# Optimization experiments

Measured on AMD Instinct MI355X. Metric: run time of the kernel, lower is better.

Reference implementation:

```python
import jax
import jax.numpy as jnp
import numpy as np

B, IN_DIM, OUT_DIM, N = 64, 1024, 512, 2048
LEAKY_SLOPE = 0.01


def apply_nl(idx, x):
    # NONLINEARITY_MAP: 0 ReLU, 1 Tanh, 2 LeakyReLU, 3 Identity, 4 Sine, 5 Softplus, 6 SoftMinus
    branches = [
        lambda v: jax.nn.relu(v),
        lambda v: jnp.tanh(v),
        lambda v: jnp.where(v >= 0, v, LEAKY_SLOPE * v),
        lambda v: v,
        lambda v: jnp.sin(v),
        lambda v: jax.nn.softplus(v),
        lambda v: -jax.nn.softplus(-v),
    ]
    return jax.lax.switch(idx, branches, x)


def setup_inputs() -> dict:
    key = jax.random.key(0)
    ks = jax.random.split(key, 8)
    X = jax.random.normal(ks[0], (B, IN_DIM), dtype=jnp.float32)
    adj = jax.random.randint(ks[1], (N, N), 0, 2).astype(bool)
    nl_idx = jax.random.randint(ks[2], (N,), 0, 7).astype(jnp.int32)
    # kaiming-normal-ish init (std = sqrt(2/fan_in)), bias std 0.1
    W0 = jax.random.normal(ks[3], (IN_DIM, N), dtype=jnp.float32) * np.sqrt(2.0 / IN_DIM)
    b0 = jax.random.normal(ks[4], (N,), dtype=jnp.float32) * 0.1
    W_mid = jax.random.normal(ks[5], (N, N), dtype=jnp.float32) * np.sqrt(2.0 / N)
    b_mid = jax.random.normal(ks[6], (N,), dtype=jnp.float32) * 0.1
    W_out = jax.random.normal(ks[7], (N, OUT_DIM), dtype=jnp.float32) * np.sqrt(2.0 / N)
    b_out = jax.random.normal(jax.random.fold_in(key, 99), (OUT_DIM,), dtype=jnp.float32) * 0.1
    return {"X": X, "adj": adj, "nl_idx": nl_idx, "W0": W0, "b0": b0,
            "W_mid": W_mid, "b_mid": b_mid, "W_out": W_out, "b_out": b_out}


def reference(X, adj, nl_idx, W0, b0, W_mid, b_mid, W_out, b_out):
    n_nodes = adj.shape[0]
    adjf = adj.astype(X.dtype)
    # node 0: Linear(input_dim, adj[0].sum()) + nonlinearity, scattered into state at adj[0]
    out0 = apply_nl(nl_idx[0], X @ W0 + b0)            # [B, N]
    state = jnp.where(adj[0][None, :], out0, jnp.zeros((), X.dtype))  # [B, N]

    # middle nodes 1..N-2: gather state[:, adj[:,n]] -> Linear(.,1) -> nonlinearity -> state[:,n]
    # gather+Linear == masked dot with full-length weight column
    def step(state, n):
        w = W_mid[:, n] * adjf[:, n]                   # [N]
        val = state @ w + b_mid[n]                     # [B]
        val = apply_nl(nl_idx[n], val)
        state = state.at[:, n].set(val)
        return state, None

    nodes = jnp.arange(1, n_nodes - 1)
    state, _ = jax.lax.scan(step, state, nodes)

    # final node: Linear(inputs.sum(), output_dim) + nonlinearity on state[:, adj[:,-1]]
    Wm = W_out * adjf[:, -1][:, None]                  # [N, OUT_DIM] masked
    out = apply_nl(nl_idx[-1], state @ Wm + b_out)     # [B, OUT_DIM]
    return out, state
```

## Files before the change

### kernel.cpp

```cpp
#include <hip/hip_runtime.h>
#include <math.h>

#define BN 64
#define KIN 1024
#define DOUT 512
#define NN 2048
#define TBLK 128
#define NBLK 16

__device__ __forceinline__ float softplus_f(float x) {
  float e = __expf(-fabsf(x));
  return fmaxf(x, 0.f) + __logf(1.f + e);
}
__device__ __forceinline__ float apply_nl(int id, float v) {
  switch (id) {
    case 0: return fmaxf(v, 0.f);
    case 1: { float e = __expf(2.f * v); return fmaf(-2.f, __builtin_amdgcn_rcpf(e + 1.f), 1.f); }
    case 2: return v >= 0.f ? v : 0.01f * v;
    case 3: return v;
    case 4: return __sinf(v);
    case 5: return softplus_f(v);
    default: return v - softplus_f(v);
  }
}

__device__ __forceinline__ void nl_cand(float v, float& mx, float& th, float& lk,
                                        float& sn, float& sp, float& sm) {
  mx = fmaxf(v, 0.f);
  lk = fmaf(fminf(v, 0.f), 0.01f, mx);
  float e = __expf(-fabsf(v));
  float e2 = e * e;
  float l1 = __logf(1.f + e);
  sp = mx + l1;
  sm = v - sp;
  th = __builtin_copysignf((1.f - e2) * __builtin_amdgcn_rcpf(1.f + e2), v);
  sn = __sinf(v);
}
__device__ __forceinline__ float nl_sel(int id, float v, float mx, float th, float lk,
                                        float sn, float sp, float sm) {
  float r = v;
  r = (id == 0) ? mx : r;
  r = (id == 1) ? th : r;
  r = (id == 2) ? lk : r;
  r = (id == 4) ? sn : r;
  r = (id == 5) ? sp : r;
  r = (id == 6) ? sm : r;
  return r;
}

#define TWEL(tw, m, l) (((l) & 3) == 0 ? tw[(m)*2 + ((l) >> 2)].x : \
                        ((l) & 3) == 1 ? tw[(m)*2 + ((l) >> 2)].y : \
                        ((l) & 3) == 2 ? tw[(m)*2 + ((l) >> 2)].z : tw[(m)*2 + ((l) >> 2)].w)

__global__ void detect_adj(const unsigned int* __restrict__ a, int* __restrict__ flags) {
  int idx = blockIdx.x * 256 + threadIdx.x;
  unsigned int v = a[idx];
  bool bad = ((v & 0xFFu) > 1u) || (((v >> 8) & 0xFFu) > 1u) ||
             (((v >> 16) & 0xFFu) > 1u) || ((v >> 24) > 1u);
  bool off = (v & 0xFFFFFF00u) != 0u;
  if (__any(bad) && (threadIdx.x & 63) == 0) atomicOr(&flags[0], 1);
  if (__any(off) && (threadIdx.x & 63) == 0) atomicOr(&flags[1], 1);
}

__global__ void normalize_adj(const unsigned char* __restrict__ a,
                              const int* __restrict__ flags,
                              unsigned char* __restrict__ out) {
  size_t i = (size_t)blockIdx.x * blockDim.x + threadIdx.x;
  int mode = flags[0] ? 2 : (flags[1] ? 1 : 0);
  unsigned char r;
  if (mode == 1)      r = (a[i] != 0);
  else if (mode == 0) r = (((const int*)a)[i] != 0);
  else                r = (((const float*)a)[i] != 0.f);
  out[i] = r;
}

__global__ void transpose_x(const float* __restrict__ X, float* __restrict__ XT) {
  int g = blockIdx.x * blockDim.x + threadIdx.x;
  int k = g >> 6, b = g & 63;
  XT[g] = X[(size_t)b * KIN + k];
}

__global__ __launch_bounds__(256) void pack_wmid(const float* __restrict__ Wmid,
                                                 const unsigned char* __restrict__ adjN,
                                                 float* __restrict__ wpack) {
  int g = blockIdx.x * 256 + threadIdx.x;
  int i = g >> 12;
  int rem = g & 4095;
  int j = rem >> 5;
  int q4 = (rem & 31) * 4;
  int n0 = 1 + i * TBLK;
  int size = NN - 1 - n0;
  if (size > TBLK) size = TBLK;
  float w[4];
#pragma unroll
  for (int e = 0; e < 4; ++e) {
    int q = q4 + e;
    float v = 0.f;
    if (q > j && j < size && q < size) {
      size_t idx = (size_t)(n0 + j) * NN + (size_t)(n0 + q);
      v = Wmid[idx] * (float)adjN[idx];
    }
    w[e] = v;
  }
  *(float4*)(wpack + (size_t)g * 4) = make_float4(w[0], w[1], w[2], w[3]);
}

template <int MODE>
__global__ __launch_bounds__(256) void gemm_partial(
    const float* __restrict__ AT, const float* __restrict__ W,
    const unsigned char* __restrict__ adj, float* __restrict__ accT,
    int ldw, int col0, int ncols, int kPerChunk, int nColTiles)
{
  const int ct = blockIdx.x % nColTiles;
  const int kc = blockIdx.x / nColTiles;
  const int c0 = ct * 64;
  const int k0 = kc * kPerChunk;
  const int t = threadIdx.x;
  const int tb = t >> 4;
  const int tc = t & 15;

  __shared__ __align__(16) float At[16][64];
  __shared__ __align__(16) float Wt[16][64];

  float acc[4][4] = {};
  const int sk = t >> 4;
  const int sq = t & 15;

  for (int ks = k0; ks < k0 + kPerChunk; ks += 16) {
    const float4 av = *(const float4*)(AT + (size_t)(ks + sk) * 64 + sq * 4);
    *(float4*)(&At[sk][sq * 4]) = av;
    {
      const float* wrow = W + (size_t)(ks + sk) * ldw + col0;
      float w[4];
      float rowmask = 1.f;
      if (MODE == 2) rowmask = (float)adj[(size_t)(ks + sk) * NN + (NN - 1)];
#pragma unroll
      for (int e = 0; e < 4; ++e) {
        int cl = c0 + sq * 4 + e;
        float wv = 0.f;
        if (cl < ncols) {
          wv = wrow[cl];
          if (MODE == 1) wv *= (float)adj[(size_t)(ks + sk) * NN + col0 + cl];
          if (MODE == 2) wv *= rowmask;
        }
        w[e] = wv;
      }
      *(float4*)(&Wt[sk][sq * 4]) = make_float4(w[0], w[1], w[2], w[3]);
    }
    __syncthreads();
#pragma unroll
    for (int kk = 0; kk < 16; ++kk) {
      float a4[4], w4[4];
#pragma unroll
      for (int e = 0; e < 4; ++e) a4[e] = At[kk][tb * 4 + e];
#pragma unroll
      for (int e = 0; e < 4; ++e) w4[e] = Wt[kk][tc * 4 + e];
#pragma unroll
      for (int i = 0; i < 4; ++i)
#pragma unroll
        for (int j = 0; j < 4; ++j) acc[i][j] = fmaf(a4[i], w4[j], acc[i][j]);
    }
    __syncthreads();
  }

#pragma unroll
  for (int j = 0; j < 4; ++j) {
    int cl = c0 + tc * 4 + j;
    if (cl < ncols) {
      float* dst = accT + (size_t)(col0 + cl) * 64 + tb * 4;
#pragma unroll
      for (int i = 0; i < 4; ++i) atomicAdd(dst + i, acc[i][j]);
    }
  }
}

__global__ void init_finish(const float* __restrict__ out0accT, const float* __restrict__ b0,
                            const unsigned char* __restrict__ adjN, const int* __restrict__ nl_idx,
                            float* __restrict__ curT) {
  int g = blockIdx.x * blockDim.x + threadIdx.x;
  int n = g >> 6;
  float v = out0accT[g] + b0[n];
  v = apply_nl(nl_idx[0], v);
  curT[g] = adjN[n] ? v : 0.f;
}

__global__ __launch_bounds__(256, 1) void fused_solve(
    const float* __restrict__ wpack, const float* __restrict__ Wmid,
    const unsigned char* __restrict__ adjN, const int* __restrict__ nlidx,
    const float* __restrict__ bmid, const float* __restrict__ Cbase,
    float* __restrict__ curT, float* __restrict__ deltaG, int* solveDone)
{
  __shared__ __align__(16) unsigned char smem[132096];
  float (*wmS)[TBLK]     = (float(*)[TBLK])(smem);
  float (*wpr)[TBLK]     = (float(*)[TBLK])(smem + 65536);
  float (*deltaFull)[64] = (float(*)[64])(smem + 65536);
  int* idS               = (int*)(smem + 131072);
  int* sfl               = (int*)(smem + 131584);

  const int bi = blockIdx.x;
  const int n0 = 1 + bi * TBLK;
  int size = NN - 1 - n0;
  if (size > TBLK) size = TBLK;
  const int tid = threadIdx.x;
  const int wv = tid >> 6;
  const int b = tid & 63;
  const int qbase = wv * 32;

  {
    const float4* src = (const float4*)(wpack + (size_t)bi * TBLK * TBLK);
    float4 s0[8];
#pragma unroll
    for (int it = 0; it < 8; ++it) s0[it] = src[it * 256 + tid];
#pragma unroll
    for (int it = 0; it < 8; ++it) ((float4*)&wmS[0][0])[it * 256 + tid] = s0[it];
#pragma unroll
    for (int it = 0; it < 8; ++it) s0[it] = src[(8 + it) * 256 + tid];
#pragma unroll
    for (int it = 0; it < 8; ++it) ((float4*)&wmS[0][0])[(8 + it) * 256 + tid] = s0[it];
  }
  if (tid < TBLK) idS[tid] = (tid < size) ? nlidx[n0 + tid] : 3;

  float val[32], iv[32];
#pragma unroll
  for (int l = 0; l < 32; ++l) {
    int q = qbase + l, n = n0 + q;
    bool ok = q < size;
    val[l] = ok ? (Cbase[(size_t)n * 64 + b] + bmid[n]) : 0.f;
    iv[l] = ok ? curT[(size_t)n * 64 + b] : 0.f;
  }
  __syncthreads();

#pragma unroll 1
  for (int p = 0; p < bi; ++p) {
    {
      const size_t rowg0 = (size_t)(1 + p * TBLK);
#pragma unroll 1
      for (int it = 0; it < 16; ++it) {
        int idx = it * 256 + tid;
        int r = idx >> 5, c4 = (idx & 31) * 4;
        const float* wrow = Wmid + (rowg0 + r) * NN + n0;
        const unsigned char* arow = adjN + (rowg0 + r) * NN + n0;
        float w[4];
#pragma unroll
        for (int e = 0; e < 4; ++e) {
          int cl = c4 + e;
          w[e] = (cl < size && arow[cl]) ? wrow[cl] : 0.f;
        }
        *(float4*)(&wpr[r][c4]) = make_float4(w[0], w[1], w[2], w[3]);
      }
    }
    {
      int done = 0, cnt = 0;
      while (!done && cnt < 4000000) {
        if (tid == 0) *sfl = atomicAdd(&solveDone[p], 0);
        __syncthreads();
        done = *sfl;
        __syncthreads();
        ++cnt;
        if (!done) __builtin_amdgcn_s_sleep(2);
      }
    }
    __threadfence();
    const float* dsrc = deltaG + (size_t)p * TBLK * 64 + b;
#pragma unroll 1
    for (int kc = 0; kc < 8; ++kc) {
      float d[16];
#pragma unroll
      for (int k = 0; k < 16; ++k) d[k] = dsrc[(size_t)(kc * 16 + k) * 64];
#pragma unroll
      for (int k = 0; k < 16; ++k) {
        const float4* wr = (const float4*)(&wpr[kc * 16 + k][qbase]);
#pragma unroll
        for (int g2 = 0; g2 < 8; ++g2) {
          float4 w4 = wr[g2];
          val[g2 * 4 + 0] = fmaf(d[k], w4.x, val[g2 * 4 + 0]);
          val[g2 * 4 + 1] = fmaf(d[k], w4.y, val[g2 * 4 + 1]);
          val[g2 * 4 + 2] = fmaf(d[k], w4.z, val[g2 * 4 + 2]);
          val[g2 * 4 + 3] = fmaf(d[k], w4.w, val[g2 * 4 + 3]);
        }
      }
    }
    __syncthreads();
  }

#pragma unroll 1
  for (int c = 0; c < 4; ++c) {
    if (wv == c) {
      const int jbase = c * 32;
      float cmx, cth, clk, csn, csp, csm;
      nl_cand(val[0], cmx, cth, clk, csn, csp, csm);
      int idv = idS[jbase];
#pragma unroll
      for (int s = 0; s < 4; ++s) {
        float4 tw[16];
#pragma unroll
        for (int m = 0; m < 8; ++m) {
          const float4* tr = (const float4*)(&wmS[jbase + s * 8 + m][qbase + s * 8]);
          tw[m * 2] = tr[0];
          tw[m * 2 + 1] = tr[1];
        }
        float ds[8];
#pragma unroll
        for (int m = 0; m < 8; ++m) {
          const int jj = s * 8 + m;
          const int j = jbase + jj;
          float nv = nl_sel(idv, val[jj], cmx, cth, clk, csn, csp, csm);
          float delta = (j < size) ? (nv - iv[jj]) : 0.f;
          ds[m] = delta;
          deltaFull[j][b] = delta;
          if (jj < 31) idv = idS[jbase + jj + 1];
          if (m < 7) {
            val[s * 8 + m + 1] = fmaf(delta, TWEL(tw, m, m + 1), val[s * 8 + m + 1]);
            nl_cand(val[s * 8 + m + 1], cmx, cth, clk, csn, csp, csm);
#pragma unroll
            for (int l = m + 2; l < 8; ++l)
              val[s * 8 + l] = fmaf(delta, TWEL(tw, m, l), val[s * 8 + l]);
          }
        }
        if (s < 3) {
#pragma unroll
          for (int lg = (s + 1) * 2; lg < 8; ++lg) {
#pragma unroll
            for (int m = 0; m < 8; ++m) {
              const float4 w4 = *(const float4*)(&wmS[jbase + s * 8 + m][qbase + lg * 4]);
              val[lg * 4 + 0] = fmaf(ds[m], w4.x, val[lg * 4 + 0]);
              val[lg * 4 + 1] = fmaf(ds[m], w4.y, val[lg * 4 + 1]);
              val[lg * 4 + 2] = fmaf(ds[m], w4.z, val[lg * 4 + 2]);
              val[lg * 4 + 3] = fmaf(ds[m], w4.w, val[lg * 4 + 3]);
            }
            if (lg == (s + 1) * 2)
              nl_cand(val[(s + 1) * 8], cmx, cth, clk, csn, csp, csm);
          }
        }
      }
    }
    __syncthreads();
    if (wv > c) {
#pragma unroll 1
      for (int jj = 0; jj < 32; ++jj) {
        const int j = c * 32 + jj;
        const float delta = deltaFull[j][b];
        const float4* wr = (const float4*)(&wmS[j][qbase]);
        float4 w0 = wr[0], w1 = wr[1], w2 = wr[2], w3 = wr[3];
        float4 w4 = wr[4], w5 = wr[5], w6 = wr[6], w7 = wr[7];
        val[0] = fmaf(delta, w0.x, val[0]);   val[1] = fmaf(delta, w0.y, val[1]);
        val[2] = fmaf(delta, w0.z, val[2]);   val[3] = fmaf(delta, w0.w, val[3]);
        val[4] = fmaf(delta, w1.x, val[4]);   val[5] = fmaf(delta, w1.y, val[5]);
        val[6] = fmaf(delta, w1.z, val[6]);   val[7] = fmaf(delta, w1.w, val[7]);
        val[8] = fmaf(delta, w2.x, val[8]);   val[9] = fmaf(delta, w2.y, val[9]);
        val[10] = fmaf(delta, w2.z, val[10]); val[11] = fmaf(delta, w2.w, val[11]);
        val[12] = fmaf(delta, w3.x, val[12]); val[13] = fmaf(delta, w3.y, val[13]);
        val[14] = fmaf(delta, w3.z, val[14]); val[15] = fmaf(delta, w3.w, val[15]);
        val[16] = fmaf(delta, w4.x, val[16]); val[17] = fmaf(delta, w4.y, val[17]);
        val[18] = fmaf(delta, w4.z, val[18]); val[19] = fmaf(delta, w4.w, val[19]);
        val[20] = fmaf(delta, w5.x, val[20]); val[21] = fmaf(delta, w5.y, val[21]);
        val[22] = fmaf(delta, w5.z, val[22]); val[23] = fmaf(delta, w5.w, val[23]);
        val[24] = fmaf(delta, w6.x, val[24]); val[25] = fmaf(delta, w6.y, val[25]);
        val[26] = fmaf(delta, w6.z, val[26]); val[27] = fmaf(delta, w6.w, val[27]);
        val[28] = fmaf(delta, w7.x, val[28]); val[29] = fmaf(delta, w7.y, val[29]);
        val[30] = fmaf(delta, w7.z, val[30]); val[31] = fmaf(delta, w7.w, val[31]);
      }
    }
    __syncthreads();
  }

  {
    const float4* sdel = (const float4*)&deltaFull[0][0];
    float4* dstD = (float4*)(deltaG + (size_t)bi * TBLK * 64);
    float4* dstC = (float4*)(curT + (size_t)n0 * 64);
#pragma unroll
    for (int it = 0; it < 8; ++it) {
      int v = it * 256 + tid;
      float4 d = sdel[v];
      dstD[v] = d;
      int r = v >> 4;
      if (r < size) {
        float4 cc = dstC[v];
        dstC[v] = make_float4(cc.x + d.x, cc.y + d.y, cc.z + d.z, cc.w + d.w);
      }
    }
  }
  __threadfence();
  __syncthreads();
  if (tid == 0) atomicExch(&solveDone[bi], 1);
}

__global__ void final_finish(const float* __restrict__ outaccT, const float* __restrict__ bout,
                             const int* __restrict__ nlidx, float* __restrict__ out) {
  int g = blockIdx.x * blockDim.x + threadIdx.x;
  int c = g >> 6, b = g & 63;
  float v = outaccT[g] + bout[c];
  v = apply_nl(nlidx[NN - 1], v);
  out[(size_t)b * DOUT + c] = v;
}

__global__ __launch_bounds__(256) void transpose_state(const float* __restrict__ curT,
                                                       float* __restrict__ stateOut) {
  __shared__ float tile[64][65];
  int n0 = blockIdx.x * 64;
  for (int r = 0; r < 16; ++r) {
    int e = r * 256 + threadIdx.x;
    tile[e >> 6][e & 63] = curT[(size_t)(n0 + (e >> 6)) * 64 + (e & 63)];
  }
  __syncthreads();
  for (int r = 0; r < 16; ++r) {
    int e = r * 256 + threadIdx.x;
    int bb = e >> 6, nn2 = e & 63;
    stateOut[(size_t)bb * NN + n0 + nn2] = tile[nn2][bb];
  }
}

extern "C" void kernel_launch(void* const* d_in, const int* in_sizes, int n_in,
                              void* d_out, int out_size, void* d_ws, size_t ws_size,
                              hipStream_t stream) {
  const float* X = (const float*)d_in[0];
  const unsigned char* adj = (const unsigned char*)d_in[1];
  const int* nl_idx = (const int*)d_in[2];
  const float* W0 = (const float*)d_in[3];
  const float* b0 = (const float*)d_in[4];
  const float* W_mid = (const float*)d_in[5];
  const float* b_mid = (const float*)d_in[6];
  const float* W_out = (const float*)d_in[7];
  const float* b_out = (const float*)d_in[8];
  float* out = (float*)d_out;
  float* stateOut = out + BN * DOUT;

  char* ws = (char*)d_ws;
  unsigned char* adjN = (unsigned char*)(ws + 0);
  int* flags = (int*)(ws + 4194304);
  float* XT = (float*)(ws + 4194560);
  float* curT = (float*)(ws + 4456704);
  float* Cbase = (float*)(ws + 4980992);
  float* out0accT = (float*)(ws + 5505280);
  float* outaccT = (float*)(ws + 6029568);
  float* wpack = (float*)(ws + 6160640);
  float* deltaG = (float*)(ws + 7209216);
  int* solveDone = flags + 8;

  hipMemsetAsync(flags, 0, 256, stream);
  hipMemsetAsync(Cbase, 0, 524288 + 524288 + 131072, stream);

  detect_adj<<<64, 256, 0, stream>>>((const unsigned int*)adj, flags);
  normalize_adj<<<16384, 256, 0, stream>>>(adj, flags, adjN);
  transpose_x<<<256, 256, 0, stream>>>(X, XT);
  pack_wmid<<<256, 256, 0, stream>>>(W_mid, adjN, wpack);

  gemm_partial<0><<<128, 256, 0, stream>>>(XT, W0, adjN, out0accT, NN, 0, NN, 256, 32);
  init_finish<<<512, 256, 0, stream>>>(out0accT, b0, adjN, nl_idx, curT);

  gemm_partial<1><<<256, 256, 0, stream>>>(curT, W_mid, adjN, Cbase, NN, 0, NN, 256, 32);

  fused_solve<<<NBLK, 256, 0, stream>>>(wpack, W_mid, adjN, nl_idx, b_mid, Cbase,
                                        curT, deltaG, solveDone);

  gemm_partial<2><<<64, 256, 0, stream>>>(curT, W_out, adjN, outaccT, DOUT, 0, DOUT, 256, 8);
  final_finish<<<128, 256, 0, stream>>>(outaccT, b_out, nl_idx, out);
  transpose_state<<<32, 256, 0, stream>>>(curT, stateOut);
}
```

Before: 870.5 us.

## Publish solved deltas per 32-row chunk to overlap inter-block dependency waits

Replaces the per-block completion flag with per-chunk flags. Each block now publishes each 32-node chunk of its solved deltas as soon as that chunk is done, and downstream blocks consume predecessor chunks as they arrive instead of waiting for the whole 128-node block. This is meant to shorten the serial critical path through the 16 chained blocks by pipelining producer and consumer work. In exchange it adds more flag polling and fences, and it shifts the workspace offsets to make room for a larger flags region.

```diff
diff --git a/kernel.cpp b/kernel.cpp
--- a/kernel.cpp
+++ b/kernel.cpp
@@ -188,7 +188,7 @@
     const float* __restrict__ wpack, const float* __restrict__ Wmid,
     const unsigned char* __restrict__ adjN, const int* __restrict__ nlidx,
     const float* __restrict__ bmid, const float* __restrict__ Cbase,
-    float* __restrict__ curT, float* __restrict__ deltaG, int* solveDone)
+    float* __restrict__ curT, float* __restrict__ deltaG, int* chunkDone)
 {
   __shared__ __align__(16) unsigned char smem[132096];
   float (*wmS)[TBLK]     = (float(*)[TBLK])(smem);
@@ -249,34 +249,34 @@
         *(float4*)(&wpr[r][c4]) = make_float4(w[0], w[1], w[2], w[3]);
       }
     }
-    {
-      int done = 0, cnt = 0;
-      while (!done && cnt < 4000000) {
-        if (tid == 0) *sfl = atomicAdd(&solveDone[p], 0);
-        __syncthreads();
-        done = *sfl;
-        __syncthreads();
-        ++cnt;
-        if (!done) __builtin_amdgcn_s_sleep(2);
-      }
-    }
-    __threadfence();
-    const float* dsrc = deltaG + (size_t)p * TBLK * 64 + b;
+    __syncthreads();
+
 #pragma unroll 1
-    for (int kc = 0; kc < 8; ++kc) {
-      float d[16];
-#pragma unroll
-      for (int k = 0; k < 16; ++k) d[k] = dsrc[(size_t)(kc * 16 + k) * 64];
-#pragma unroll
-      for (int k = 0; k < 16; ++k) {
-        const float4* wr = (const float4*)(&wpr[kc * 16 + k][qbase]);
+    for (int c2 = 0; c2 < 4; ++c2) {
+      {
+        int done = 0, cnt = 0;
+        while (!done && cnt < 4000000) {
+          if (tid == 0) *sfl = atomicAdd(&chunkDone[p * 4 + c2], 0);
+          __syncthreads();
+          done = *sfl;
+          __syncthreads();
+          ++cnt;
+          if (!done) __builtin_amdgcn_s_sleep(2);
+        }
+      }
+      __threadfence();
+      const float* dsrc = deltaG + ((size_t)p * TBLK + c2 * 32) * 64 + b;
+#pragma unroll
+      for (int r = 0; r < 32; ++r) {
+        const float d = dsrc[(size_t)r * 64];
+        const float4* wr = (const float4*)(&wpr[c2 * 32 + r][qbase]);
 #pragma unroll
         for (int g2 = 0; g2 < 8; ++g2) {
           float4 w4 = wr[g2];
-          val[g2 * 4 + 0] = fmaf(d[k], w4.x, val[g2 * 4 + 0]);
-          val[g2 * 4 + 1] = fmaf(d[k], w4.y, val[g2 * 4 + 1]);
-          val[g2 * 4 + 2] = fmaf(d[k], w4.z, val[g2 * 4 + 2]);
-          val[g2 * 4 + 3] = fmaf(d[k], w4.w, val[g2 * 4 + 3]);
+          val[g2 * 4 + 0] = fmaf(d, w4.x, val[g2 * 4 + 0]);
+          val[g2 * 4 + 1] = fmaf(d, w4.y, val[g2 * 4 + 1]);
+          val[g2 * 4 + 2] = fmaf(d, w4.z, val[g2 * 4 + 2]);
+          val[g2 * 4 + 3] = fmaf(d, w4.w, val[g2 * 4 + 3]);
         }
       }
     }
@@ -335,30 +335,27 @@
       }
     }
     __syncthreads();
-    if (wv > c) {
-#pragma unroll 1
+    if (wv == c) {
+      const float4* sdel = (const float4*)(&deltaFull[c * 32][0]);
+      float4* dstD = (float4*)(deltaG + ((size_t)bi * TBLK + c * 32) * 64);
+#pragma unroll
+      for (int it = 0; it < 8; ++it) dstD[it * 64 + b] = sdel[it * 64 + b];
+      __threadfence();
+      if (b == 0) atomicExch(&chunkDone[bi * 4 + c], 1);
+    } else if (wv > c) {
+#pragma unroll
       for (int jj = 0; jj < 32; ++jj) {
         const int j = c * 32 + jj;
         const float delta = deltaFull[j][b];
         const float4* wr = (const float4*)(&wmS[j][qbase]);
-        float4 w0 = wr[0], w1 = wr[1], w2 = wr[2], w3 = wr[3];
-        float4 w4 = wr[4], w5 = wr[5], w6 = wr[6], w7 = wr[7];
-        val[0] = fmaf(delta, w0.x, val[0]);   val[1] = fmaf(delta, w0.y, val[1]);
-        val[2] = fmaf(delta, w0.z, val[2]);   val[3] = fmaf(delta, w0.w, val[3]);
-        val[4] = fmaf(delta, w1.x, val[4]);   val[5] = fmaf(delta, w1.y, val[5]);
-        val[6] = fmaf(delta, w1.z, val[6]);   val[7] = fmaf(delta, w1.w, val[7]);
-        val[8] = fmaf(delta, w2.x, val[8]);   val[9] = fmaf(delta, w2.y, val[9]);
-        val[10] = fmaf(delta, w2.z, val[10]); val[11] = fmaf(delta, w2.w, val[11]);
-        val[12] = fmaf(delta, w3.x, val[12]); val[13] = fmaf(delta, w3.y, val[13]);
-        val[14] = fmaf(delta, w3.z, val[14]); val[15] = fmaf(delta, w3.w, val[15]);
-        val[16] = fmaf(delta, w4.x, val[16]); val[17] = fmaf(delta, w4.y, val[17]);
-        val[18] = fmaf(delta, w4.z, val[18]); val[19] = fmaf(delta, w4.w, val[19]);
-        val[20] = fmaf(delta, w5.x, val[20]); val[21] = fmaf(delta, w5.y, val[21]);
-        val[22] = fmaf(delta, w5.z, val[22]); val[23] = fmaf(delta, w5.w, val[23]);
-        val[24] = fmaf(delta, w6.x, val[24]); val[25] = fmaf(delta, w6.y, val[25]);
-        val[26] = fmaf(delta, w6.z, val[26]); val[27] = fmaf(delta, w6.w, val[27]);
-        val[28] = fmaf(delta, w7.x, val[28]); val[29] = fmaf(delta, w7.y, val[29]);
-        val[30] = fmaf(delta, w7.z, val[30]); val[31] = fmaf(delta, w7.w, val[31]);
+#pragma unroll
+        for (int g2 = 0; g2 < 8; ++g2) {
+          float4 w4 = wr[g2];
+          val[g2 * 4 + 0] = fmaf(delta, w4.x, val[g2 * 4 + 0]);
+          val[g2 * 4 + 1] = fmaf(delta, w4.y, val[g2 * 4 + 1]);
+          val[g2 * 4 + 2] = fmaf(delta, w4.z, val[g2 * 4 + 2]);
+          val[g2 * 4 + 3] = fmaf(delta, w4.w, val[g2 * 4 + 3]);
+        }
       }
     }
     __syncthreads();
@@ -366,23 +363,18 @@
 
   {
     const float4* sdel = (const float4*)&deltaFull[0][0];
-    float4* dstD = (float4*)(deltaG + (size_t)bi * TBLK * 64);
     float4* dstC = (float4*)(curT + (size_t)n0 * 64);
 #pragma unroll
     for (int it = 0; it < 8; ++it) {
       int v = it * 256 + tid;
-      float4 d = sdel[v];
-      dstD[v] = d;
       int r = v >> 4;
       if (r < size) {
+        float4 d = sdel[v];
         float4 cc = dstC[v];
         dstC[v] = make_float4(cc.x + d.x, cc.y + d.y, cc.z + d.z, cc.w + d.w);
       }
     }
   }
-  __threadfence();
-  __syncthreads();
-  if (tid == 0) atomicExch(&solveDone[bi], 1);
 }
 
 __global__ void final_finish(const float* __restrict__ outaccT, const float* __restrict__ bout,
@@ -428,16 +420,16 @@
   char* ws = (char*)d_ws;
   unsigned char* adjN = (unsigned char*)(ws + 0);
   int* flags = (int*)(ws + 4194304);
-  float* XT = (float*)(ws + 4194560);
-  float* curT = (float*)(ws + 4456704);
-  float* Cbase = (float*)(ws + 4980992);
-  float* out0accT = (float*)(ws + 5505280);
-  float* outaccT = (float*)(ws + 6029568);
-  float* wpack = (float*)(ws + 6160640);
-  float* deltaG = (float*)(ws + 7209216);
-  int* solveDone = flags + 8;
-
-  hipMemsetAsync(flags, 0, 256, stream);
+  float* XT = (float*)(ws + 4194816);
+  float* curT = (float*)(ws + 4456960);
+  float* Cbase = (float*)(ws + 4981248);
+  float* out0accT = (float*)(ws + 5505536);
+  float* outaccT = (float*)(ws + 6029824);
+  float* wpack = (float*)(ws + 6160896);
+  float* deltaG = (float*)(ws + 7209472);
+  int* chunkDone = flags + 8;
+
+  hipMemsetAsync(flags, 0, 512, stream);
   hipMemsetAsync(Cbase, 0, 524288 + 524288 + 131072, stream);
 
   detect_adj<<<64, 256, 0, stream>>>((const unsigned int*)adj, flags);
@@ -451,7 +443,7 @@
   gemm_partial<1><<<256, 256, 0, stream>>>(curT, W_mid, adjN, Cbase, NN, 0, NN, 256, 32);
 
   fused_solve<<<NBLK, 256, 0, stream>>>(wpack, W_mid, adjN, nl_idx, b_mid, Cbase,
-                                        curT, deltaG, solveDone);
+                                        curT, deltaG, chunkDone);
 
   gemm_partial<2><<<64, 256, 0, stream>>>(curT, W_out, adjN, outaccT, DOUT, 0, DOUT, 256, 8);
   final_finish<<<128, 256, 0, stream>>>(outaccT, b_out, nl_idx, out);
```

Result: faster. 726.9 us (-16.5%).
